# Kernel optimization log

Measured on AMD Instinct MI355X. Metric: run time of the kernel, lower is better.

## Reference

```python
import jax, jax.numpy as jnp
import numpy as np

DIM = 2048
RANK = 16
NUM_EXPERTS = 8


def setup_inputs() -> dict:
    key = jax.random.key(0)
    ks = jax.random.split(key, 8)
    x = jax.random.normal(ks[0], (4, 2048, DIM), dtype=jnp.float32)
    # router gate: nn.Linear(dim, num_experts) -> weight [E, dim], bias [E]
    gate_w = jax.random.normal(ks[1], (NUM_EXPERTS, DIM), dtype=jnp.float32) * 0.02
    gate_b = jnp.zeros((NUM_EXPERTS,), dtype=jnp.float32)
    # base_ffn: nn.Linear(dim, dim) -> weight [dim, dim], bias [dim]
    base_w = jax.random.normal(ks[2], (DIM, DIM), dtype=jnp.float32) * 0.02
    base_b = jnp.zeros((DIM,), dtype=jnp.float32)
    # LoRA experts, stacked: A maps dim->rank, B maps rank->dim (stored input-major)
    lora_A = jax.random.normal(ks[3], (NUM_EXPERTS, DIM, RANK), dtype=jnp.float32) * 0.02
    lora_B = jax.random.normal(ks[4], (NUM_EXPERTS, RANK, DIM), dtype=jnp.float32) * 0.02
    return {"x": x, "gate_w": gate_w, "gate_b": gate_b,
            "base_w": base_w, "base_b": base_b,
            "lora_A": lora_A, "lora_B": lora_B}


def reference(x, gate_w, gate_b, base_w, base_b, lora_A, lora_B):
    B, S, D = x.shape
    flat = x.reshape(-1, D)  # [T, D]
    # base FFN: Linear + exact GELU (torch default)
    base_out = jax.nn.gelu(flat @ base_w.T + base_b, approximate=False)
    # router: softmax then top-1
    probs = jax.nn.softmax(flat @ gate_w.T + gate_b, axis=-1)  # [T, E]
    idx = jnp.argmax(probs, axis=-1)                            # [T] top-1 index
    w = jnp.take_along_axis(probs, idx[:, None], axis=-1)      # [T, 1] top-1 weight
    E = lora_A.shape[0]
    expert_out = jnp.zeros_like(flat)
    for e in range(E):  # fixed small expert loop; GEMMs are dense over all tokens
        h = jax.nn.gelu(flat @ lora_A[e], approximate=False)   # [T, rank]
        ye = h @ lora_B[e]                                      # [T, D]
        sel = (idx == e)[:, None]
        expert_out = expert_out + jnp.where(sel, ye * w, 0.0)
    out = (base_out + expert_out).reshape(B, S, D)
    return out, probs
```

## Files before the change

### kernel.cpp

```cpp
#include <hip/hip_runtime.h>
#include <hip/hip_bf16.h>
#include <math.h>


#define DIM   2048
#define RANK  16
#define NEXP  8
#define NTOK  8192
#define KLORA 128

typedef __hip_bfloat16 bf16;
typedef __attribute__((ext_vector_type(8))) short short8;
typedef __attribute__((ext_vector_type(4))) float float4v;

typedef const __attribute__((address_space(1))) void* gptr_t;
typedef __attribute__((address_space(3))) void*       sptr_t;

__device__ __forceinline__ void async_ld16(const bf16* g, bf16* l) {
    __builtin_amdgcn_global_load_lds((gptr_t)g, (sptr_t)l, 16, 0, 0);
}

__device__ __forceinline__ float gelu_fast(float x) {
    float t = 0.7978845608028654f * (x + 0.044715f * x * x * x);
    t = fminf(fmaxf(t, -10.0f), 10.0f);
    float e = __expf(2.0f * t);
    float th = (e - 1.0f) / (e + 1.0f);
    return 0.5f * x * (1.0f + th);
}

__device__ __forceinline__ short8 pack8(float4 v0, float4 v1) {
    union { bf16 h[8]; short8 v; } u;
    u.h[0] = __float2bfloat16(v0.x); u.h[1] = __float2bfloat16(v0.y);
    u.h[2] = __float2bfloat16(v0.z); u.h[3] = __float2bfloat16(v0.w);
    u.h[4] = __float2bfloat16(v1.x); u.h[5] = __float2bfloat16(v1.y);
    u.h[6] = __float2bfloat16(v1.z); u.h[7] = __float2bfloat16(v1.w);
    return u.v;
}

__global__ __launch_bounds__(256) void cvt_logits_kernel(
    const float* __restrict__ x, const float* __restrict__ gate_w,
    const float* __restrict__ gate_b, const float* __restrict__ base_w,
    const float* __restrict__ lora_B, const float* __restrict__ lora_A,
    bf16* __restrict__ Xb, bf16* __restrict__ Wb,
    bf16* __restrict__ Bt, bf16* __restrict__ Ab,
    float* __restrict__ probs, int* __restrict__ idx_out, float* __restrict__ w_out)
{
    __shared__ float buf[2560];
    const int b   = blockIdx.x;
    const int tid = threadIdx.x;

    if (b < 1024) {
        const int t0 = b * 8;
        float4 g0[NEXP], g1[NEXP];
        #pragma unroll
        for (int e = 0; e < NEXP; e++) {
            const float* wr = gate_w + (size_t)e * DIM + tid * 8;
            g0[e] = *(const float4*)wr;
            g1[e] = *(const float4*)(wr + 4);
        }
        const int wave = tid >> 6, lane = tid & 63;
        const int eown = ((lane & 1) << 2) | (lane & 2) | ((lane & 4) >> 2);
        #pragma unroll
        for (int tt = 0; tt < 8; tt++) {
            const int t = t0 + tt;
            const float* xr = x + (size_t)t * DIM + tid * 8;
            float4 v0 = *(const float4*)xr;
            float4 v1 = *(const float4*)(xr + 4);
            *(short8*)(Xb + (size_t)t * DIM + tid * 8) = pack8(v0, v1);
            float a[NEXP];
            #pragma unroll
            for (int e = 0; e < NEXP; e++) {
                a[e] = v0.x * g0[e].x + v0.y * g0[e].y + v0.z * g0[e].z + v0.w * g0[e].w
                     + v1.x * g1[e].x + v1.y * g1[e].y + v1.z * g1[e].z + v1.w * g1[e].w;
            }
            float b4[4];
            #pragma unroll
            for (int i = 0; i < 4; i++) {
                float send = (lane & 1) ? a[i]     : a[i + 4];
                float keep = (lane & 1) ? a[i + 4] : a[i];
                b4[i] = keep + __shfl_xor(send, 1);
            }
            float b2[2];
            #pragma unroll
            for (int i = 0; i < 2; i++) {
                float send = (lane & 2) ? b4[i]     : b4[i + 2];
                float keep = (lane & 2) ? b4[i + 2] : b4[i];
                b2[i] = keep + __shfl_xor(send, 2);
            }
            float send3 = (lane & 4) ? b2[0] : b2[1];
            float keep3 = (lane & 4) ? b2[1] : b2[0];
            float s = keep3 + __shfl_xor(send3, 4);
            s += __shfl_xor(s, 8);
            s += __shfl_xor(s, 16);
            s += __shfl_xor(s, 32);
            if (lane < NEXP) buf[tt * 32 + wave * NEXP + eown] = s;
        }
        __syncthreads();
        if (tid < 8) {
            const int t = t0 + tid;
            float l[NEXP]; float mx = -1e30f;
            #pragma unroll
            for (int e = 0; e < NEXP; e++) {
                l[e] = buf[tid * 32 + e] + buf[tid * 32 + 8 + e]
                     + buf[tid * 32 + 16 + e] + buf[tid * 32 + 24 + e] + gate_b[e];
                mx = fmaxf(mx, l[e]);
            }
            float sum = 0.f;
            #pragma unroll
            for (int e = 0; e < NEXP; e++) { l[e] = __expf(l[e] - mx); sum += l[e]; }
            float inv = 1.0f / sum;
            int es = 0; float best = l[0];
            #pragma unroll
            for (int e = 1; e < NEXP; e++) if (l[e] > best) { best = l[e]; es = e; }
            #pragma unroll
            for (int e = 0; e < NEXP; e++) probs[(size_t)t * NEXP + e] = l[e] * inv;
            idx_out[t] = es;
            w_out[t]   = best * inv;
        }
    } else if (b < 1024 + 2048) {
        size_t v = ((size_t)(b - 1024) * 256 + tid) * 8;
        float4 v0 = *(const float4*)(base_w + v);
        float4 v1 = *(const float4*)(base_w + v + 4);
        *(short8*)(Wb + v) = pack8(v0, v1);
    } else if (b < 1024 + 2048 + 256) {
        int bb = b - 1024 - 2048;
        int kk0 = (bb >> 6) * 32, j0 = (bb & 63) * 32;
        {
            int r = tid >> 3, c4 = (tid & 7) * 4;
            float4 val = *(const float4*)(lora_B + (size_t)(kk0 + r) * DIM + j0 + c4);
            *(float4*)(buf + r * 36 + c4) = val;
        }
        __syncthreads();
        {
            int j = tid >> 3, k4 = (tid & 7) * 4;
            bf16* dst = Bt + (size_t)(j0 + j) * KLORA + kk0 + k4;
            #pragma unroll
            for (int i = 0; i < 4; i++) dst[i] = __float2bfloat16(buf[(k4 + i) * 36 + j]);
        }
    } else {
        int bb = b - 1024 - 2048 - 256;
        int e = bb >> 4, k0 = (bb & 15) * 128;
        const float* src = lora_A + (size_t)e * DIM * RANK;
        {
            int k = tid >> 2, r4 = (tid & 3) * 4;
            float4 va = *(const float4*)(src + (size_t)(k0 + k) * RANK + r4);
            float4 vb = *(const float4*)(src + (size_t)(k0 + k + 64) * RANK + r4);
            *(float4*)(buf + k * 20 + r4)        = va;
            *(float4*)(buf + (k + 64) * 20 + r4) = vb;
        }
        __syncthreads();
        {
            int r = tid >> 4, kx = (tid & 15) * 8;
            bf16* dst = Ab + (size_t)(e * 16 + r) * DIM + k0 + kx;
            #pragma unroll
            for (int i = 0; i < 8; i++) dst[i] = __float2bfloat16(buf[(kx + i) * 20 + r]);
        }
    }
}

__global__ __launch_bounds__(256) void hsel_kernel(
    const bf16* __restrict__ Xb, const bf16* __restrict__ Ab,
    const int* __restrict__ idx, const float* __restrict__ wsel,
    bf16* __restrict__ A2)
{
    __shared__ bf16 As[4 * 32 * 64];
    __shared__ bf16 Bs[4 * 64 * 64];
    const int tid  = threadIdx.x;
    const int wave = tid >> 6, lane = tid & 63;
    const int m0 = blockIdx.x * 32;
    const int n0 = blockIdx.y * 64;
    const int col = lane & 15, quad = lane >> 4;

    const int kc = ((tid & 7) ^ ((tid >> 3) & 7)) * 8;
    const int sr = tid >> 3;
    const bf16* gA  = Xb + (size_t)(m0 + sr) * DIM + kc;
    const bf16* gB0 = Ab + (size_t)(n0 + sr) * DIM + kc;
    const bf16* gB1 = gB0 + (size_t)32 * DIM;
    bf16* lA = As + wave * 512;
    bf16* lB = Bs + wave * 512;

    int slot[2];
    #pragma unroll
    for (int p = 0; p < 2; p++)
        slot[p] = (((p << 2) | quad) ^ (col & 7)) * 8;
    const bf16* pa = As + col * 64;
    const bf16* pb = Bs + (wave * 16 + col) * 64;

    float4v acc[2] = {};
    for (int k0 = 0; k0 < DIM; k0 += 256) {
        __syncthreads();
        #pragma unroll
        for (int h = 0; h < 4; h++) {
            async_ld16(gA  + k0 + h * 64, lA + h * 2048);
            async_ld16(gB0 + k0 + h * 64, lB + h * 4096);
            async_ld16(gB1 + k0 + h * 64, lB + h * 4096 + 2048);
        }
        __syncthreads();
        #pragma unroll
        for (int ks = 0; ks < 8; ks++) {
            const int h = ks >> 1, p = ks & 1;
            short8 a0 = *(const short8*)(pa + h * 2048 + slot[p]);
            short8 a1 = *(const short8*)(pa + h * 2048 + 1024 + slot[p]);
            short8 b0 = *(const short8*)(pb + h * 4096 + slot[p]);
            acc[0] = __builtin_amdgcn_mfma_f32_16x16x32_bf16(a0, b0, acc[0], 0, 0, 0);
            acc[1] = __builtin_amdgcn_mfma_f32_16x16x32_bf16(a1, b0, acc[1], 0, 0, 0);
        }
    }

    const int jcol = n0 + wave * 16 + col;
    const int ej   = jcol >> 4;
    #pragma unroll
    for (int i = 0; i < 2; i++) {
        int rbase = m0 + i * 16 + quad * 4;
        #pragma unroll
        for (int r = 0; r < 4; r++) {
            int t = rbase + r;
            float v = (idx[t] == ej) ? gelu_fast(acc[i][r]) * wsel[t] : 0.0f;
            A2[(size_t)t * KLORA + jcol] = __float2bfloat16(v);
        }
    }
}

__global__ __launch_bounds__(256, 3) void gemm_kernel(
    const bf16* __restrict__ Xb, const bf16* __restrict__ Wb,
    const float* __restrict__ base_b,
    const bf16* __restrict__ A2, const bf16* __restrict__ Bt,
    float* __restrict__ out)
{
    __shared__ bf16 As[128 * 64];
    __shared__ bf16 Bs[128 * 64];
    const int tid  = threadIdx.x;
    const int wave = tid >> 6, lane = tid & 63;
    const int wm = wave >> 1, wn = wave & 1;
    const int m0 = blockIdx.x * 128;
    const int n0 = blockIdx.y * 128;
    const int col = lane & 15, quad = lane >> 4;

    const int kc = (((tid & 7) ^ ((tid >> 3) & 7))) * 8;
    const int r0 = tid >> 3;
    const bf16* gA0 = Xb + (size_t)(m0 + r0) * DIM + kc;
    const bf16* gB0 = Wb + (size_t)(n0 + r0) * DIM + kc;
    const bf16* gA1 = gA0 + (size_t)32 * DIM;
    const bf16* gB1 = gB0 + (size_t)32 * DIM;
    const bf16* gA2 = gA0 + (size_t)64 * DIM;
    const bf16* gB2 = gB0 + (size_t)64 * DIM;
    const bf16* gA3 = gA0 + (size_t)96 * DIM;
    const bf16* gB3 = gB0 + (size_t)96 * DIM;
    bf16* lA = As + wave * 512;
    bf16* lB = Bs + wave * 512;

    const int sl0 = (quad        ^ (col & 7)) * 8;
    const int sl1 = ((quad | 4)  ^ (col & 7)) * 8;
    const bf16* paA = As + (wm * 64 + col) * 64;
    const bf16* pbB = Bs + (wn * 64 + col) * 64;

    float4v acc[4][4] = {};

    for (int k0 = 0; k0 < DIM; k0 += 64) {
        __syncthreads();
        async_ld16(gA0 + k0, lA);
        async_ld16(gA1 + k0, lA + 2048);
        async_ld16(gA2 + k0, lA + 4096);
        async_ld16(gA3 + k0, lA + 6144);
        async_ld16(gB0 + k0, lB);
        async_ld16(gB1 + k0, lB + 2048);
        async_ld16(gB2 + k0, lB + 4096);
        async_ld16(gB3 + k0, lB + 6144);
        __syncthreads();
        {
            short8 a[4], b[4];
            #pragma unroll
            for (int i = 0; i < 4; i++) a[i] = *(const short8*)(paA + i * 1024 + sl0);
            #pragma unroll
            for (int j = 0; j < 4; j++) b[j] = *(const short8*)(pbB + j * 1024 + sl0);
            #pragma unroll
            for (int i = 0; i < 4; i++)
                #pragma unroll
                for (int j = 0; j < 4; j++)
                    acc[i][j] = __builtin_amdgcn_mfma_f32_16x16x32_bf16(
                        a[i], b[j], acc[i][j], 0, 0, 0);
        }
        {
            short8 a[4], b[4];
            #pragma unroll
            for (int i = 0; i < 4; i++) a[i] = *(const short8*)(paA + i * 1024 + sl1);
            #pragma unroll
            for (int j = 0; j < 4; j++) b[j] = *(const short8*)(pbB + j * 1024 + sl1);
            #pragma unroll
            for (int i = 0; i < 4; i++)
                #pragma unroll
                for (int j = 0; j < 4; j++)
                    acc[i][j] = __builtin_amdgcn_mfma_f32_16x16x32_bf16(
                        a[i], b[j], acc[i][j], 0, 0, 0);
        }
    }

    float bias[4];
    #pragma unroll
    for (int j = 0; j < 4; j++) bias[j] = base_b[n0 + wn * 64 + j * 16 + col];
    #pragma unroll
    for (int i = 0; i < 4; i++)
        #pragma unroll
        for (int j = 0; j < 4; j++)
            #pragma unroll
            for (int r = 0; r < 4; r++)
                acc[i][j][r] = gelu_fast(acc[i][j][r] + bias[j]);

    const bf16* pea = A2 + (size_t)(m0 + wm * 64 + col) * KLORA + quad * 8;
    const bf16* peb = Bt + (size_t)(n0 + wn * 64 + col) * KLORA + quad * 8;
    #pragma unroll
    for (int ks = 0; ks < 4; ks++) {
        short8 ea[4], eb[4];
        #pragma unroll
        for (int i = 0; i < 4; i++)
            ea[i] = *(const short8*)(pea + i * 16 * KLORA + ks * 32);
        #pragma unroll
        for (int j = 0; j < 4; j++)
            eb[j] = *(const short8*)(peb + j * 16 * KLORA + ks * 32);
        #pragma unroll
        for (int i = 0; i < 4; i++)
            #pragma unroll
            for (int j = 0; j < 4; j++)
                acc[i][j] = __builtin_amdgcn_mfma_f32_16x16x32_bf16(
                    ea[i], eb[j], acc[i][j], 0, 0, 0);
    }

    #pragma unroll
    for (int i = 0; i < 4; i++) {
        #pragma unroll
        for (int j = 0; j < 4; j++) {
            int tt = m0 + wm * 64 + i * 16 + quad * 4;
            int jj = n0 + wn * 64 + j * 16 + col;
            float* po = out + (size_t)tt * DIM + jj;
            #pragma unroll
            for (int r = 0; r < 4; r++) po[(size_t)r * DIM] = acc[i][j][r];
        }
    }
}

extern "C" void kernel_launch(void* const* d_in, const int* in_sizes, int n_in,
                              void* d_out, int out_size, void* d_ws, size_t ws_size,
                              hipStream_t stream)
{
    (void)in_sizes; (void)n_in; (void)out_size; (void)ws_size;
    const float* x      = (const float*)d_in[0];
    const float* gate_w = (const float*)d_in[1];
    const float* gate_b = (const float*)d_in[2];
    const float* base_w = (const float*)d_in[3];
    const float* base_b = (const float*)d_in[4];
    const float* lora_A = (const float*)d_in[5];
    const float* lora_B = (const float*)d_in[6];

    float* out   = (float*)d_out;
    float* probs = out + (size_t)NTOK * DIM;

    char* ws = (char*)d_ws;
    bf16*  Xb   = (bf16*)ws;
    bf16*  Wb   = (bf16*)(ws + 33554432);
    bf16*  A2   = (bf16*)(ws + 41943040);
    bf16*  Bt   = (bf16*)(ws + 44040192);
    bf16*  Ab   = (bf16*)(ws + 44564480);
    int*   idx  = (int*) (ws + 45088768);
    float* wsel = (float*)(ws + 45121536);

    cvt_logits_kernel<<<1024 + 2048 + 256 + 128, 256, 0, stream>>>(
        x, gate_w, gate_b, base_w, lora_B, lora_A,
        Xb, Wb, Bt, Ab, probs, idx, wsel);
    hsel_kernel<<<dim3(256, 2), 256, 0, stream>>>(Xb, Ab, idx, wsel, A2);
    gemm_kernel<<<dim3(64, 16), 256, 0, stream>>>(Xb, Wb, base_b, A2, Bt, out);
}
```

Baseline: 243.7 us.

## Move base_w and lora_B conversion into hsel kernel; raise gemm occupancy

Moves the base_w fp32-to-bf16 conversion and the lora_B transpose out of the first kernel and into the second (the LoRA hidden-selection kernel) as extra block ranges. This shortens the critical first kernel and lets the memory-bound conversions run alongside the small compute-bound hsel blocks. It also raises the gemm launch_bounds minimum to 4 blocks per SM and recomputes the load addresses inline to cut register pressure. The risk is register spills in the gemm at higher occupancy, and less even load balance in the merged kernel.

```diff
diff --git a/kernel.cpp b/kernel.cpp
--- a/kernel.cpp
+++ b/kernel.cpp
@@ -39,10 +39,8 @@
 
 __global__ __launch_bounds__(256) void cvt_logits_kernel(
     const float* __restrict__ x, const float* __restrict__ gate_w,
-    const float* __restrict__ gate_b, const float* __restrict__ base_w,
-    const float* __restrict__ lora_B, const float* __restrict__ lora_A,
-    bf16* __restrict__ Xb, bf16* __restrict__ Wb,
-    bf16* __restrict__ Bt, bf16* __restrict__ Ab,
+    const float* __restrict__ gate_b, const float* __restrict__ lora_A,
+    bf16* __restrict__ Xb, bf16* __restrict__ Ab,
     float* __restrict__ probs, int* __restrict__ idx_out, float* __restrict__ w_out)
 {
     __shared__ float buf[2560];
@@ -117,28 +115,8 @@
             idx_out[t] = es;
             w_out[t]   = best * inv;
         }
-    } else if (b < 1024 + 2048) {
-        size_t v = ((size_t)(b - 1024) * 256 + tid) * 8;
-        float4 v0 = *(const float4*)(base_w + v);
-        float4 v1 = *(const float4*)(base_w + v + 4);
-        *(short8*)(Wb + v) = pack8(v0, v1);
-    } else if (b < 1024 + 2048 + 256) {
-        int bb = b - 1024 - 2048;
-        int kk0 = (bb >> 6) * 32, j0 = (bb & 63) * 32;
-        {
-            int r = tid >> 3, c4 = (tid & 7) * 4;
-            float4 val = *(const float4*)(lora_B + (size_t)(kk0 + r) * DIM + j0 + c4);
-            *(float4*)(buf + r * 36 + c4) = val;
-        }
-        __syncthreads();
-        {
-            int j = tid >> 3, k4 = (tid & 7) * 4;
-            bf16* dst = Bt + (size_t)(j0 + j) * KLORA + kk0 + k4;
-            #pragma unroll
-            for (int i = 0; i < 4; i++) dst[i] = __float2bfloat16(buf[(k4 + i) * 36 + j]);
-        }
     } else {
-        int bb = b - 1024 - 2048 - 256;
+        int bb = b - 1024;
         int e = bb >> 4, k0 = (bb & 15) * 128;
         const float* src = lora_A + (size_t)e * DIM * RANK;
         {
@@ -158,70 +136,96 @@
     }
 }
 
-__global__ __launch_bounds__(256) void hsel_kernel(
+__global__ __launch_bounds__(256) void hselx_kernel(
     const bf16* __restrict__ Xb, const bf16* __restrict__ Ab,
     const int* __restrict__ idx, const float* __restrict__ wsel,
-    bf16* __restrict__ A2)
+    const float* __restrict__ base_w, const float* __restrict__ lora_B,
+    bf16* __restrict__ A2, bf16* __restrict__ Wb, bf16* __restrict__ Bt)
 {
     __shared__ bf16 As[4 * 32 * 64];
     __shared__ bf16 Bs[4 * 64 * 64];
-    const int tid  = threadIdx.x;
-    const int wave = tid >> 6, lane = tid & 63;
-    const int m0 = blockIdx.x * 32;
-    const int n0 = blockIdx.y * 64;
-    const int col = lane & 15, quad = lane >> 4;
-
-    const int kc = ((tid & 7) ^ ((tid >> 3) & 7)) * 8;
-    const int sr = tid >> 3;
-    const bf16* gA  = Xb + (size_t)(m0 + sr) * DIM + kc;
-    const bf16* gB0 = Ab + (size_t)(n0 + sr) * DIM + kc;
-    const bf16* gB1 = gB0 + (size_t)32 * DIM;
-    bf16* lA = As + wave * 512;
-    bf16* lB = Bs + wave * 512;
-
-    int slot[2];
-    #pragma unroll
-    for (int p = 0; p < 2; p++)
-        slot[p] = (((p << 2) | quad) ^ (col & 7)) * 8;
-    const bf16* pa = As + col * 64;
-    const bf16* pb = Bs + (wave * 16 + col) * 64;
-
-    float4v acc[2] = {};
-    for (int k0 = 0; k0 < DIM; k0 += 256) {
-        __syncthreads();
-        #pragma unroll
-        for (int h = 0; h < 4; h++) {
-            async_ld16(gA  + k0 + h * 64, lA + h * 2048);
-            async_ld16(gB0 + k0 + h * 64, lB + h * 4096);
-            async_ld16(gB1 + k0 + h * 64, lB + h * 4096 + 2048);
-        }
-        __syncthreads();
-        #pragma unroll
-        for (int ks = 0; ks < 8; ks++) {
-            const int h = ks >> 1, p = ks & 1;
-            short8 a0 = *(const short8*)(pa + h * 2048 + slot[p]);
-            short8 a1 = *(const short8*)(pa + h * 2048 + 1024 + slot[p]);
-            short8 b0 = *(const short8*)(pb + h * 4096 + slot[p]);
-            acc[0] = __builtin_amdgcn_mfma_f32_16x16x32_bf16(a0, b0, acc[0], 0, 0, 0);
-            acc[1] = __builtin_amdgcn_mfma_f32_16x16x32_bf16(a1, b0, acc[1], 0, 0, 0);
-        }
-    }
-
-    const int jcol = n0 + wave * 16 + col;
-    const int ej   = jcol >> 4;
-    #pragma unroll
-    for (int i = 0; i < 2; i++) {
-        int rbase = m0 + i * 16 + quad * 4;
-        #pragma unroll
-        for (int r = 0; r < 4; r++) {
-            int t = rbase + r;
-            float v = (idx[t] == ej) ? gelu_fast(acc[i][r]) * wsel[t] : 0.0f;
-            A2[(size_t)t * KLORA + jcol] = __float2bfloat16(v);
-        }
-    }
-}
-
-__global__ __launch_bounds__(256, 3) void gemm_kernel(
+    float* buf = (float*)As;
+    const int bid = blockIdx.x;
+    const int tid = threadIdx.x;
+
+    if (bid < 512) {
+        const int wave = tid >> 6, lane = tid & 63;
+        const int m0 = (bid & 255) * 32;
+        const int n0 = (bid >> 8) * 64;
+        const int col = lane & 15, quad = lane >> 4;
+
+        const int kc = ((tid & 7) ^ ((tid >> 3) & 7)) * 8;
+        const int sr = tid >> 3;
+        const bf16* gA  = Xb + (size_t)(m0 + sr) * DIM + kc;
+        const bf16* gB0 = Ab + (size_t)(n0 + sr) * DIM + kc;
+        const bf16* gB1 = gB0 + (size_t)32 * DIM;
+        bf16* lA = As + wave * 512;
+        bf16* lB = Bs + wave * 512;
+
+        int slot[2];
+        #pragma unroll
+        for (int p = 0; p < 2; p++)
+            slot[p] = (((p << 2) | quad) ^ (col & 7)) * 8;
+        const bf16* pa = As + col * 64;
+        const bf16* pb = Bs + (wave * 16 + col) * 64;
+
+        float4v acc[2] = {};
+        for (int k0 = 0; k0 < DIM; k0 += 256) {
+            __syncthreads();
+            #pragma unroll
+            for (int h = 0; h < 4; h++) {
+                async_ld16(gA  + k0 + h * 64, lA + h * 2048);
+                async_ld16(gB0 + k0 + h * 64, lB + h * 4096);
+                async_ld16(gB1 + k0 + h * 64, lB + h * 4096 + 2048);
+            }
+            __syncthreads();
+            #pragma unroll
+            for (int ks = 0; ks < 8; ks++) {
+                const int h = ks >> 1, p = ks & 1;
+                short8 a0 = *(const short8*)(pa + h * 2048 + slot[p]);
+                short8 a1 = *(const short8*)(pa + h * 2048 + 1024 + slot[p]);
+                short8 b0 = *(const short8*)(pb + h * 4096 + slot[p]);
+                acc[0] = __builtin_amdgcn_mfma_f32_16x16x32_bf16(a0, b0, acc[0], 0, 0, 0);
+                acc[1] = __builtin_amdgcn_mfma_f32_16x16x32_bf16(a1, b0, acc[1], 0, 0, 0);
+            }
+        }
+
+        const int jcol = n0 + wave * 16 + col;
+        const int ej   = jcol >> 4;
+        #pragma unroll
+        for (int i = 0; i < 2; i++) {
+            int rbase = m0 + i * 16 + quad * 4;
+            #pragma unroll
+            for (int r = 0; r < 4; r++) {
+                int t = rbase + r;
+                float v = (idx[t] == ej) ? gelu_fast(acc[i][r]) * wsel[t] : 0.0f;
+                A2[(size_t)t * KLORA + jcol] = __float2bfloat16(v);
+            }
+        }
+    } else if (bid < 512 + 2048) {
+        size_t v = ((size_t)(bid - 512) * 256 + tid) * 8;
+        float4 v0 = *(const float4*)(base_w + v);
+        float4 v1 = *(const float4*)(base_w + v + 4);
+        *(short8*)(Wb + v) = pack8(v0, v1);
+    } else {
+        int bb = bid - 512 - 2048;
+        int kk0 = (bb >> 6) * 32, j0 = (bb & 63) * 32;
+        {
+            int r = tid >> 3, c4 = (tid & 7) * 4;
+            float4 val = *(const float4*)(lora_B + (size_t)(kk0 + r) * DIM + j0 + c4);
+            *(float4*)(buf + r * 36 + c4) = val;
+        }
+        __syncthreads();
+        {
+            int j = tid >> 3, k4 = (tid & 7) * 4;
+            bf16* dst = Bt + (size_t)(j0 + j) * KLORA + kk0 + k4;
+            #pragma unroll
+            for (int i = 0; i < 4; i++) dst[i] = __float2bfloat16(buf[(k4 + i) * 36 + j]);
+        }
+    }
+}
+
+__global__ __launch_bounds__(256, 4) void gemm_kernel(
     const bf16* __restrict__ Xb, const bf16* __restrict__ Wb,
     const float* __restrict__ base_b,
     const bf16* __restrict__ A2, const bf16* __restrict__ Bt,
@@ -240,12 +244,6 @@
     const int r0 = tid >> 3;
     const bf16* gA0 = Xb + (size_t)(m0 + r0) * DIM + kc;
     const bf16* gB0 = Wb + (size_t)(n0 + r0) * DIM + kc;
-    const bf16* gA1 = gA0 + (size_t)32 * DIM;
-    const bf16* gB1 = gB0 + (size_t)32 * DIM;
-    const bf16* gA2 = gA0 + (size_t)64 * DIM;
-    const bf16* gB2 = gB0 + (size_t)64 * DIM;
-    const bf16* gA3 = gA0 + (size_t)96 * DIM;
-    const bf16* gB3 = gB0 + (size_t)96 * DIM;
     bf16* lA = As + wave * 512;
     bf16* lB = Bs + wave * 512;
 
@@ -258,14 +256,16 @@
 
     for (int k0 = 0; k0 < DIM; k0 += 64) {
         __syncthreads();
-        async_ld16(gA0 + k0, lA);
-        async_ld16(gA1 + k0, lA + 2048);
-        async_ld16(gA2 + k0, lA + 4096);
-        async_ld16(gA3 + k0, lA + 6144);
-        async_ld16(gB0 + k0, lB);
-        async_ld16(gB1 + k0, lB + 2048);
-        async_ld16(gB2 + k0, lB + 4096);
-        async_ld16(gB3 + k0, lB + 6144);
+        const bf16* ga = gA0 + k0;
+        const bf16* gb = gB0 + k0;
+        async_ld16(ga,                       lA);
+        async_ld16(ga + (size_t)32 * DIM,    lA + 2048);
+        async_ld16(ga + (size_t)64 * DIM,    lA + 4096);
+        async_ld16(ga + (size_t)96 * DIM,    lA + 6144);
+        async_ld16(gb,                       lB);
+        async_ld16(gb + (size_t)32 * DIM,    lB + 2048);
+        async_ld16(gb + (size_t)64 * DIM,    lB + 4096);
+        async_ld16(gb + (size_t)96 * DIM,    lB + 6144);
         __syncthreads();
         {
             short8 a[4], b[4];
@@ -363,9 +363,9 @@
     int*   idx  = (int*) (ws + 45088768);
     float* wsel = (float*)(ws + 45121536);
 
-    cvt_logits_kernel<<<1024 + 2048 + 256 + 128, 256, 0, stream>>>(
-        x, gate_w, gate_b, base_w, lora_B, lora_A,
-        Xb, Wb, Bt, Ab, probs, idx, wsel);
-    hsel_kernel<<<dim3(256, 2), 256, 0, stream>>>(Xb, Ab, idx, wsel, A2);
+    cvt_logits_kernel<<<1024 + 128, 256, 0, stream>>>(
+        x, gate_w, gate_b, lora_A, Xb, Ab, probs, idx, wsel);
+    hselx_kernel<<<512 + 2048 + 256, 256, 0, stream>>>(
+        Xb, Ab, idx, wsel, base_w, lora_B, A2, Wb, Bt);
     gemm_kernel<<<dim3(64, 16), 256, 0, stream>>>(Xb, Wb, base_b, A2, Bt, out);
 }
```

Result: slower. 251.6 us (+3.2%).
